# Kernel optimization log

Measured on AMD Instinct MI355X. Metric: run time of the kernel, lower is better.

## Reference

```python
import jax, jax.numpy as jnp
import numpy as np

N = 20000       # nodes
E = 320000      # edges (before self-loops)
F_IN = 128
HID = 128
HEADS = 4
OUT_DIM = 2
B = 64          # graphs in batch
SLOPE = 0.2     # GATv2 leaky_relu negative slope (PyG default)


def _glorot(key, shape):
    fan_in, fan_out = shape[0], shape[1]
    limit = np.sqrt(6.0 / (fan_in + fan_out)).astype(np.float32)
    return jax.random.uniform(key, shape, jnp.float32, -limit, limit)


def setup_inputs() -> dict:
    key = jax.random.key(0)
    ks = jax.random.split(key, 24)
    inp = {
        'x': jax.random.normal(ks[0], (N, F_IN), jnp.float32),
        'edge_src': jax.random.randint(ks[1], (E,), 0, N),
        'edge_dst': jax.random.randint(ks[2], (E,), 0, N),
        'batch': jnp.sort(jax.random.randint(ks[3], (N,), 0, B)),
        # layer 1: in=F_IN, out=HEADS*HID, concat
        'Wl1': _glorot(ks[4], (F_IN, HEADS * HID)),
        'Wr1': _glorot(ks[5], (F_IN, HEADS * HID)),
        'bl1': jnp.zeros((HEADS * HID,), jnp.float32),
        'br1': jnp.zeros((HEADS * HID,), jnp.float32),
        'att1': _glorot(ks[6], (HEADS, HID)),
        'bias1': jnp.zeros((HEADS * HID,), jnp.float32),
        # layer 2: in=HEADS*HID, out=HEADS*HID, concat
        'Wl2': _glorot(ks[7], (HEADS * HID, HEADS * HID)),
        'Wr2': _glorot(ks[8], (HEADS * HID, HEADS * HID)),
        'bl2': jnp.zeros((HEADS * HID,), jnp.float32),
        'br2': jnp.zeros((HEADS * HID,), jnp.float32),
        'att2': _glorot(ks[9], (HEADS, HID)),
        'bias2': jnp.zeros((HEADS * HID,), jnp.float32),
        # layer 3: in=HEADS*HID, heads=1, concat=False -> out=HID
        'Wl3': _glorot(ks[10], (HEADS * HID, HID)),
        'Wr3': _glorot(ks[11], (HEADS * HID, HID)),
        'bl3': jnp.zeros((HID,), jnp.float32),
        'br3': jnp.zeros((HID,), jnp.float32),
        'att3': _glorot(ks[12], (1, HID)),
        'bias3': jnp.zeros((HID,), jnp.float32),
        # output MLP
        'W_mlp1': _glorot(ks[13], (HID, HID)),
        'b_mlp1': jnp.zeros((HID,), jnp.float32),
        'W_mlp2': _glorot(ks[14], (HID, OUT_DIM)),
        'b_mlp2': jnp.zeros((OUT_DIM,), jnp.float32),
    }
    return inp


def gatv2_layer(x, src, dst, Wl, Wr, bl, br, att, bias, concat):
    """PyG GATv2Conv (eval mode): alpha_ij = softmax_j over N(i) of a^T LeakyReLU(xl_j + xr_i)."""
    H, C = att.shape
    n = x.shape[0]
    xl = (x @ Wl + bl).reshape(n, H, C)   # source transform
    e = jax.nn.leaky_relu(xl[src] + (x @ Wr + br).reshape(n, H, C)[dst], SLOPE)  # [E,H,C]
    logits = jnp.einsum('ehc,hc->eh', e, att)                                    # [E,H]
    # segment softmax over destination node
    m = jax.ops.segment_max(logits, dst, num_segments=n)
    alpha = jnp.exp(logits - m[dst])
    denom = jax.ops.segment_sum(alpha, dst, num_segments=n)
    alpha = alpha / denom[dst]
    out = jax.ops.segment_sum(xl[src] * alpha[..., None], dst, num_segments=n)   # [N,H,C]
    out = out.reshape(n, H * C) if concat else out.mean(axis=1)
    return out + bias


def reference(x, edge_src, edge_dst, batch,
              Wl1, Wr1, bl1, br1, att1, bias1,
              Wl2, Wr2, bl2, br2, att2, bias2,
              Wl3, Wr3, bl3, br3, att3, bias3,
              W_mlp1, b_mlp1, W_mlp2, b_mlp2):
    n = x.shape[0]
    loop = jnp.arange(n, dtype=edge_src.dtype)
    src = jnp.concatenate([edge_src, loop])   # PyG add_self_loops=True
    dst = jnp.concatenate([edge_dst, loop])

    h = jax.nn.elu(gatv2_layer(x, src, dst, Wl1, Wr1, bl1, br1, att1, bias1, True))
    h = jax.nn.elu(gatv2_layer(h, src, dst, Wl2, Wr2, bl2, br2, att2, bias2, True))
    h = jax.nn.elu(gatv2_layer(h, src, dst, Wl3, Wr3, bl3, br3, att3, bias3, False))

    # global_mean_pool over graph ids
    counts = jnp.maximum(jax.ops.segment_sum(jnp.ones((n,), h.dtype), batch, num_segments=B), 1.0)
    pooled = jax.ops.segment_sum(h, batch, num_segments=B) / counts[:, None]

    hidden = jax.nn.relu(pooled @ W_mlp1 + b_mlp1)
    return hidden @ W_mlp2 + b_mlp2
```

## Files before the change

### kernel.cpp

```cpp
#include <hip/hip_runtime.h>
#include <math.h>


typedef __attribute__((ext_vector_type(4))) float f32x4;
typedef __attribute__((ext_vector_type(8))) _Float16 f16x8;
typedef __attribute__((ext_vector_type(4))) _Float16 f16x4;
typedef __attribute__((ext_vector_type(2))) _Float16 f16x2;

__device__ __forceinline__ float elu1(float x) {
    return (x > 0.f) ? x : (__expf(x) - 1.f);
}
__device__ __forceinline__ f16x2 pk_leaky(f16x2 s) {
    const f16x2 slope = {(_Float16)0.2f, (_Float16)0.2f};
    return __builtin_elementwise_max(s, s * slope);
}

__global__ void zero32_kernel(int* __restrict__ p, int n) {
    int i = blockIdx.x * 256 + threadIdx.x;
    if (i < n) p[i] = 0;
}

__global__ void count_kernel(const int* __restrict__ dst, int* __restrict__ cnt,
                             int E, int N) {
    int e = blockIdx.x * 256 + threadIdx.x;
    if (e < E + N) {
        int d = (e < E) ? dst[e] : (e - E);
        atomicAdd(&cnt[d], 1);
    }
}

__global__ __launch_bounds__(1024) void scan_kernel(const int* __restrict__ cnt,
                                                    int* __restrict__ rowstart,
                                                    int* __restrict__ cursor,
                                                    int N, int total) {
    __shared__ int part[1024];
    int t = threadIdx.x;
    int ch = (N + 1023) >> 10;
    int base = t * ch;
    int loc[32];
    int s = 0;
    for (int i = 0; i < ch && i < 32; ++i) {
        int idx = base + i;
        int v = (idx < N) ? cnt[idx] : 0;
        loc[i] = s;
        s += v;
    }
    part[t] = s;
    __syncthreads();
    for (int off = 1; off < 1024; off <<= 1) {
        int v = (t >= off) ? part[t - off] : 0;
        __syncthreads();
        part[t] += v;
        __syncthreads();
    }
    int excl = (t == 0) ? 0 : part[t - 1];
    for (int i = 0; i < ch && i < 32; ++i) {
        int idx = base + i;
        if (idx < N) {
            int v = excl + loc[i];
            rowstart[idx] = v;
            cursor[idx]   = v;
        }
    }
    if (t == 0) rowstart[N] = total;
}

__global__ void scatter_kernel(const int* __restrict__ src, const int* __restrict__ dst,
                               int* __restrict__ cursor, int* __restrict__ csr_src,
                               int E, int N) {
    int e = blockIdx.x * 256 + threadIdx.x;
    if (e < E + N) {
        int d, s;
        if (e < E) { d = dst[e]; s = src[e]; }
        else       { d = e - E; s = e - E; }
        int pos = atomicAdd(&cursor[d], 1);
        csr_src[pos] = s;
    }
}

__global__ void boundary_kernel(const int* __restrict__ batch,
                                int* __restrict__ gstart, int N, int B) {
    int n = blockIdx.x * 256 + threadIdx.x;
    if (n > N) return;
    int cur  = (n < N) ? batch[n] : B;
    int prev = (n == 0) ? -1 : batch[n - 1];
    for (int g = prev + 1; g <= cur; ++g) gstart[g] = n;
}

__global__ void convA_kernel(const float* __restrict__ X, _Float16* __restrict__ A,
                             int n_valid, int n_total) {
    int i = (blockIdx.x * 256 + threadIdx.x) * 4;
    if (i >= n_total) return;
    float4 v = (i < n_valid) ? *(const float4*)(X + i) : make_float4(0.f, 0.f, 0.f, 0.f);
    f16x4 h;
    h.x = (_Float16)v.x; h.y = (_Float16)v.y;
    h.z = (_Float16)v.z; h.w = (_Float16)v.w;
    *(f16x4*)(A + i) = h;
}

__global__ __launch_bounds__(256) void convWT_kernel(
    const float* __restrict__ Wl, const float* __restrict__ Wr,
    _Float16* __restrict__ Bth, _Float16* __restrict__ Btl, int K, int Nh) {
    __shared__ float tile[32][33];
    int kb = blockIdx.x * 32;
    int nb = blockIdx.y * 32;
    int tx = threadIdx.x;
    int ty = threadIdx.y;
#pragma unroll
    for (int j = 0; j < 4; ++j) {
        int kk = kb + ty + j * 8;
        int nn = nb + tx;
        float v = (nn < Nh) ? Wl[(size_t)kk * Nh + nn]
                            : Wr[(size_t)kk * Nh + (nn - Nh)];
        tile[ty + j * 8][tx] = v;
    }
    __syncthreads();
#pragma unroll
    for (int j = 0; j < 4; ++j) {
        int nn = nb + ty + j * 8;
        int kk = kb + tx;
        float v = tile[tx][ty + j * 8];
        _Float16 h = (_Float16)v;
        Bth[(size_t)nn * K + kk] = h;
        Btl[(size_t)nn * K + kk] = (_Float16)(v - (float)h);
    }
}

#define SCW 132
__global__ __launch_bounds__(256, 1) void gemm_f16_kernel(
    const _Float16* __restrict__ A,
    const _Float16* __restrict__ Bh, const _Float16* __restrict__ Bl,
    const float* __restrict__ biasL, const float* __restrict__ biasR, int Nh_,
    _Float16* __restrict__ P, _Float16* __restrict__ Q, int K, int NT) {
    __shared__ __align__(16) char smem[49152];
    float* sC = (float*)(smem);

    const int tid  = threadIdx.x;
    const int lane = tid & 63;
    const int wv   = tid >> 6;
    const int wm   = wv & 1;
    const int wn   = wv >> 1;
    const int fm   = lane & 15;
    const int q    = lane >> 4;

    const int bi = blockIdx.x;
    const int kx = bi & 7;
    const int tt = bi >> 3;
    const int m0 = ((tt / NT) * 8 + kx) * 128;
    const int n0 = (tt % NT) * 128;

    const int r0  = lane >> 2;
    const int kco = (lane & 3) << 3;

    f32x4 acc[4][4];
#pragma unroll
    for (int i = 0; i < 4; ++i)
#pragma unroll
        for (int j = 0; j < 4; ++j) {
            acc[i][j].x = 0.f; acc[i][j].y = 0.f;
            acc[i][j].z = 0.f; acc[i][j].w = 0.f;
        }

    const int nIters = K >> 5;
    int cur = 0;
    {
        char* base = smem;
#pragma unroll
        for (int j = 0; j < 2; ++j) {
            int wc  = wv * 2 + j;
            int row = wc * 16 + r0;
            size_t ga = (size_t)(m0 + row) * K + kco;
            size_t gb = (size_t)(n0 + row) * K + kco;
            int lofs = wc * 1024;
            __builtin_amdgcn_global_load_lds(
                (const __attribute__((address_space(1))) void*)(A + ga),
                (__attribute__((address_space(3))) void*)(base + lofs), 16, 0, 0);
            __builtin_amdgcn_global_load_lds(
                (const __attribute__((address_space(1))) void*)(Bh + gb),
                (__attribute__((address_space(3))) void*)(base + 8192 + lofs), 16, 0, 0);
            __builtin_amdgcn_global_load_lds(
                (const __attribute__((address_space(1))) void*)(Bl + gb),
                (__attribute__((address_space(3))) void*)(base + 16384 + lofs), 16, 0, 0);
        }
    }
    for (int it = 0; it < nIters; ++it) {
        __syncthreads();
        if (it + 1 < nIters) {
            char* base = smem + (cur ^ 1) * 24576;
            int ks = (it + 1) << 5;
#pragma unroll
            for (int j = 0; j < 2; ++j) {
                int wc  = wv * 2 + j;
                int row = wc * 16 + r0;
                size_t ga = (size_t)(m0 + row) * K + ks + kco;
                size_t gb = (size_t)(n0 + row) * K + ks + kco;
                int lofs = wc * 1024;
                __builtin_amdgcn_global_load_lds(
                    (const __attribute__((address_space(1))) void*)(A + ga),
                    (__attribute__((address_space(3))) void*)(base + lofs), 16, 0, 0);
                __builtin_amdgcn_global_load_lds(
                    (const __attribute__((address_space(1))) void*)(Bh + gb),
                    (__attribute__((address_space(3))) void*)(base + 8192 + lofs), 16, 0, 0);
                __builtin_amdgcn_global_load_lds(
                    (const __attribute__((address_space(1))) void*)(Bl + gb),
                    (__attribute__((address_space(3))) void*)(base + 16384 + lofs), 16, 0, 0);
            }
        }

        _Float16* cA  = (_Float16*)(smem + cur * 24576);
        _Float16* cBh = (_Float16*)(smem + cur * 24576 + 8192);
        _Float16* cBl = (_Float16*)(smem + cur * 24576 + 16384);
        f16x8 ah[4];
#pragma unroll
        for (int mi = 0; mi < 4; ++mi)
            ah[mi] = *(const f16x8*)&cA[(wm * 64 + mi * 16 + fm) * 32 + q * 8];
#pragma unroll
        for (int ni = 0; ni < 4; ++ni) {
            int r = (wn * 64 + ni * 16 + fm) * 32 + q * 8;
            f16x8 bh = *(const f16x8*)&cBh[r];
            f16x8 bl = *(const f16x8*)&cBl[r];
#pragma unroll
            for (int mi = 0; mi < 4; ++mi) {
                acc[mi][ni] = __builtin_amdgcn_mfma_f32_16x16x32_f16(ah[mi], bh, acc[mi][ni], 0, 0, 0);
                acc[mi][ni] = __builtin_amdgcn_mfma_f32_16x16x32_f16(ah[mi], bl, acc[mi][ni], 0, 0, 0);
            }
        }
        cur ^= 1;
    }

    float bsv[4];
#pragma unroll
    for (int ni = 0; ni < 4; ++ni) {
        int col = n0 + wn * 64 + ni * 16 + fm;
        bsv[ni] = (col < Nh_) ? biasL[col] : biasR[col - Nh_];
    }

    _Float16* dstbase = (n0 < Nh_) ? P : Q;
    const int col0 = (n0 < Nh_) ? n0 : (n0 - Nh_);

#pragma unroll
    for (int c = 0; c < 2; ++c) {
        __syncthreads();
        if (wm == c) {
#pragma unroll
            for (int mi = 0; mi < 4; ++mi)
#pragma unroll
                for (int ni = 0; ni < 4; ++ni) {
                    int base = (mi * 16 + q * 4) * SCW + wn * 64 + ni * 16 + fm;
                    sC[base]           = acc[mi][ni].x + bsv[ni];
                    sC[base + SCW]     = acc[mi][ni].y + bsv[ni];
                    sC[base + 2 * SCW] = acc[mi][ni].z + bsv[ni];
                    sC[base + 3 * SCW] = acc[mi][ni].w + bsv[ni];
                }
        }
        __syncthreads();
#pragma unroll
        for (int j = 0; j < 8; ++j) {
            int flat = j * 256 + tid;
            int row  = flat >> 5;
            int col  = (flat & 31) * 4;
            f32x4 v = *(const f32x4*)(sC + row * SCW + col);
            f16x4 hv;
            hv.x = (_Float16)v.x; hv.y = (_Float16)v.y;
            hv.z = (_Float16)v.z; hv.w = (_Float16)v.w;
            *(f16x4*)(dstbase + (size_t)(m0 + c * 64 + row) * Nh_ + col0 + col) = hv;
        }
    }
}

__global__ __launch_bounds__(256) void gat_edge4_kernel(
    const _Float16* __restrict__ P, const _Float16* __restrict__ Q,
    const float* __restrict__ att, const float* __restrict__ bias,
    const int* __restrict__ rowstart, const int* __restrict__ srcs,
    _Float16* __restrict__ H, int N) {
    __shared__ float s_l[4][4];
    __shared__ float s_acc[4][512];

    int n = blockIdx.x;
    int wv = threadIdx.x >> 6;
    int lane = threadIdx.x & 63;
    int c0 = lane * 8;
    int h = lane >> 4;

    f16x8 rv = *(const f16x8*)(Q + (size_t)n * 512 + c0);
    f16x2 r2[4], t2[4];
#pragma unroll
    for (int k = 0; k < 4; ++k) {
        r2[k].x = rv[2 * k]; r2[k].y = rv[2 * k + 1];
        t2[k].x = (_Float16)att[c0 + 2 * k];
        t2[k].y = (_Float16)att[c0 + 2 * k + 1];
    }

    float acc[8];
#pragma unroll
    for (int j = 0; j < 8; ++j) acc[j] = 0.f;
    float l_run = 0.f;

    int beg = rowstart[n], end = rowstart[n + 1];
    int i = beg + wv * 2;
    for (; i + 1 < end; i += 8) {
        int s0 = srcs[i];
        int s1 = srcs[i + 1];
        f16x8 hv0 = *(const f16x8*)(P + (size_t)s0 * 512 + c0);
        f16x8 hv1 = *(const f16x8*)(P + (size_t)s1 * 512 + c0);
        float p0 = 0.f, p1 = 0.f;
#pragma unroll
        for (int k = 0; k < 4; ++k) {
            f16x2 a0; a0.x = hv0[2 * k]; a0.y = hv0[2 * k + 1];
            f16x2 a1; a1.x = hv1[2 * k]; a1.y = hv1[2 * k + 1];
            p0 = __builtin_amdgcn_fdot2(pk_leaky(a0 + r2[k]), t2[k], p0, false);
            p1 = __builtin_amdgcn_fdot2(pk_leaky(a1 + r2[k]), t2[k], p1, false);
        }
        p0 += __shfl_xor(p0, 1, 16);
        p1 += __shfl_xor(p1, 1, 16);
        p0 += __shfl_xor(p0, 2, 16);
        p1 += __shfl_xor(p1, 2, 16);
        p0 += __shfl_xor(p0, 4, 16);
        p1 += __shfl_xor(p1, 4, 16);
        p0 += __shfl_xor(p0, 8, 16);
        p1 += __shfl_xor(p1, 8, 16);
        float w0 = __expf(p0);
        float w1 = __expf(p1);
        l_run += w0 + w1;
#pragma unroll
        for (int j = 0; j < 8; ++j) {
            float a = fmaf((float)hv0[j], w0, acc[j]);
            acc[j] = fmaf((float)hv1[j], w1, a);
        }
    }
    if (i < end) {
        int s = srcs[i];
        f16x8 hv = *(const f16x8*)(P + (size_t)s * 512 + c0);
        float p = 0.f;
#pragma unroll
        for (int k = 0; k < 4; ++k) {
            f16x2 a; a.x = hv[2 * k]; a.y = hv[2 * k + 1];
            p = __builtin_amdgcn_fdot2(pk_leaky(a + r2[k]), t2[k], p, false);
        }
        p += __shfl_xor(p, 1, 16);
        p += __shfl_xor(p, 2, 16);
        p += __shfl_xor(p, 4, 16);
        p += __shfl_xor(p, 8, 16);
        float w = __expf(p);
        l_run += w;
#pragma unroll
        for (int j = 0; j < 8; ++j)
            acc[j] = fmaf((float)hv[j], w, acc[j]);
    }
    if ((lane & 15) == 0) s_l[wv][h] = l_run;
    *(float4*)&s_acc[wv][c0]     = make_float4(acc[0], acc[1], acc[2], acc[3]);
    *(float4*)&s_acc[wv][c0 + 4] = make_float4(acc[4], acc[5], acc[6], acc[7]);
    __syncthreads();
    if (wv == 0) {
        float L = s_l[0][h] + s_l[1][h] + s_l[2][h] + s_l[3][h];
        float o[8];
#pragma unroll
        for (int j = 0; j < 8; ++j) o[j] = 0.f;
#pragma unroll
        for (int w = 0; w < 4; ++w) {
            float4 q0 = *(const float4*)&s_acc[w][c0];
            float4 q1 = *(const float4*)&s_acc[w][c0 + 4];
            o[0] += q0.x; o[1] += q0.y; o[2] += q0.z; o[3] += q0.w;
            o[4] += q1.x; o[5] += q1.y; o[6] += q1.z; o[7] += q1.w;
        }
        float inv = 1.f / L;
        f16x8 oh;
#pragma unroll
        for (int j = 0; j < 8; ++j)
            oh[j] = (_Float16)elu1(o[j] * inv + bias[c0 + j]);
        *(f16x8*)(H + (size_t)n * 512 + c0) = oh;
    }
}

__global__ __launch_bounds__(256) void gat_edge1_kernel(
    const _Float16* __restrict__ P, const _Float16* __restrict__ Q,
    const float* __restrict__ att, const float* __restrict__ bias,
    const int* __restrict__ rowstart, const int* __restrict__ srcs,
    float* __restrict__ out, int N) {
    __shared__ float s_l[4];
    __shared__ float s_acc[4][128];

    int n = blockIdx.x;
    int wv = threadIdx.x >> 6;
    int lane = threadIdx.x & 63;
    int c0 = lane * 2;

    f16x2 rv = *(const f16x2*)(Q + (size_t)n * 128 + c0);
    f16x2 t2;
    t2.x = (_Float16)att[c0];
    t2.y = (_Float16)att[c0 + 1];

    float acc0 = 0.f, acc1 = 0.f;
    float l_run = 0.f;

    int beg = rowstart[n], end = rowstart[n + 1];
    int i = beg + wv * 2;
    for (; i + 1 < end; i += 8) {
        int s0 = srcs[i];
        int s1 = srcs[i + 1];
        f16x2 h0 = *(const f16x2*)(P + (size_t)s0 * 128 + c0);
        f16x2 h1 = *(const f16x2*)(P + (size_t)s1 * 128 + c0);
        float p0 = __builtin_amdgcn_fdot2(pk_leaky(h0 + rv), t2, 0.f, false);
        float p1 = __builtin_amdgcn_fdot2(pk_leaky(h1 + rv), t2, 0.f, false);
        p0 += __shfl_xor(p0, 1, 64);
        p1 += __shfl_xor(p1, 1, 64);
        p0 += __shfl_xor(p0, 2, 64);
        p1 += __shfl_xor(p1, 2, 64);
        p0 += __shfl_xor(p0, 4, 64);
        p1 += __shfl_xor(p1, 4, 64);
        p0 += __shfl_xor(p0, 8, 64);
        p1 += __shfl_xor(p1, 8, 64);
        p0 += __shfl_xor(p0, 16, 64);
        p1 += __shfl_xor(p1, 16, 64);
        p0 += __shfl_xor(p0, 32, 64);
        p1 += __shfl_xor(p1, 32, 64);
        float w0 = __expf(p0);
        float w1 = __expf(p1);
        l_run += w0 + w1;
        acc0 = fmaf((float)h1.x, w1, fmaf((float)h0.x, w0, acc0));
        acc1 = fmaf((float)h1.y, w1, fmaf((float)h0.y, w0, acc1));
    }
    if (i < end) {
        int s = srcs[i];
        f16x2 hv = *(const f16x2*)(P + (size_t)s * 128 + c0);
        float p = __builtin_amdgcn_fdot2(pk_leaky(hv + rv), t2, 0.f, false);
        p += __shfl_xor(p, 1, 64);
        p += __shfl_xor(p, 2, 64);
        p += __shfl_xor(p, 4, 64);
        p += __shfl_xor(p, 8, 64);
        p += __shfl_xor(p, 16, 64);
        p += __shfl_xor(p, 32, 64);
        float w = __expf(p);
        l_run += w;
        acc0 = fmaf((float)hv.x, w, acc0);
        acc1 = fmaf((float)hv.y, w, acc1);
    }
    if (lane == 0) s_l[wv] = l_run;
    *(float2*)&s_acc[wv][c0] = make_float2(acc0, acc1);
    __syncthreads();
    if (wv == 0) {
        float L = s_l[0] + s_l[1] + s_l[2] + s_l[3];
        float o0 = 0.f, o1 = 0.f;
#pragma unroll
        for (int w = 0; w < 4; ++w) {
            float2 qv = *(const float2*)&s_acc[w][c0];
            o0 += qv.x;
            o1 += qv.y;
        }
        float inv = 1.f / L;
        float2 w2;
        w2.x = elu1(o0 * inv + bias[c0]);
        w2.y = elu1(o1 * inv + bias[c0 + 1]);
        *(float2*)(out + (size_t)n * 128 + c0) = w2;
    }
}

__global__ __launch_bounds__(256) void pool2_kernel(
    const float* __restrict__ h3, const int* __restrict__ gstart,
    float* __restrict__ pooled) {
    __shared__ float red[256];
    int g = blockIdx.x;
    int c = threadIdx.x & 127;
    int h = threadIdx.x >> 7;
    int gs = gstart[g], ge = gstart[g + 1];
    float s = 0.f;
    for (int n = gs + h; n < ge; n += 2) s += h3[(size_t)n * 128 + c];
    red[threadIdx.x] = s;
    __syncthreads();
    if (h == 0) {
        float tot = red[c] + red[c + 128];
        float cnt = fmaxf((float)(ge - gs), 1.f);
        pooled[g * 128 + c] = tot / cnt;
    }
}

__global__ __launch_bounds__(128) void mlp_kernel(
    const float* __restrict__ pooled,
    const float* __restrict__ W1, const float* __restrict__ b1,
    const float* __restrict__ W2, const float* __restrict__ b2,
    float* __restrict__ out) {
    __shared__ float pr[128];
    __shared__ float2 red[128];
    int g = blockIdx.x;
    int t = threadIdx.x;
    pr[t] = pooled[g * 128 + t];
    __syncthreads();
    float h = b1[t];
#pragma unroll 4
    for (int k = 0; k < 128; ++k) h = fmaf(pr[k], W1[k * 128 + t], h);
    h = fmaxf(h, 0.0f);
    red[t] = make_float2(h * W2[t * 2], h * W2[t * 2 + 1]);
    __syncthreads();
    for (int s = 64; s > 0; s >>= 1) {
        if (t < s) {
            red[t].x += red[t + s].x;
            red[t].y += red[t + s].y;
        }
        __syncthreads();
    }
    if (t == 0) {
        out[g * 2]     = red[0].x + b2[0];
        out[g * 2 + 1] = red[0].y + b2[1];
    }
}

extern "C" void kernel_launch(void* const* d_in, const int* in_sizes, int n_in,
                              void* d_out, int out_size, void* d_ws, size_t ws_size,
                              hipStream_t stream) {
    const float* x     = (const float*)d_in[0];
    const int*   esrc  = (const int*)d_in[1];
    const int*   edst  = (const int*)d_in[2];
    const int*   batch = (const int*)d_in[3];
    const float* Wl1   = (const float*)d_in[4];
    const float* Wr1   = (const float*)d_in[5];
    const float* bl1   = (const float*)d_in[6];
    const float* br1   = (const float*)d_in[7];
    const float* att1  = (const float*)d_in[8];
    const float* bias1 = (const float*)d_in[9];
    const float* Wl2   = (const float*)d_in[10];
    const float* Wr2   = (const float*)d_in[11];
    const float* bl2   = (const float*)d_in[12];
    const float* br2   = (const float*)d_in[13];
    const float* att2  = (const float*)d_in[14];
    const float* bias2 = (const float*)d_in[15];
    const float* Wl3   = (const float*)d_in[16];
    const float* Wr3   = (const float*)d_in[17];
    const float* bl3   = (const float*)d_in[18];
    const float* br3   = (const float*)d_in[19];
    const float* att3  = (const float*)d_in[20];
    const float* bias3 = (const float*)d_in[21];
    const float* Wm1   = (const float*)d_in[22];
    const float* bm1   = (const float*)d_in[23];
    const float* Wm2   = (const float*)d_in[24];
    const float* bm2   = (const float*)d_in[25];

    int N  = in_sizes[0] / 128;
    int E  = in_sizes[1];
    int ET = E + N;
    int B  = out_size / 2;
    const int Mp = 160 * 128;

    char* ws = (char*)d_ws;
    size_t off = 0;
    auto alloc = [&](size_t bytes) -> void* {
        void* p = ws + off;
        off += (bytes + 255) & ~(size_t)255;
        return p;
    };
    _Float16* P    = (_Float16*)alloc((size_t)Mp * 512 * 2);
    _Float16* Q    = (_Float16*)alloc((size_t)Mp * 512 * 2);
    _Float16* A1   = (_Float16*)alloc((size_t)Mp * 128 * 2);
    _Float16* Hb   = (_Float16*)alloc((size_t)Mp * 512 * 2);
    _Float16* Wth1 = (_Float16*)alloc((size_t)1024 * 128 * 2);
    _Float16* Wtl1 = (_Float16*)alloc((size_t)1024 * 128 * 2);
    _Float16* Wth2 = (_Float16*)alloc((size_t)1024 * 512 * 2);
    _Float16* Wtl2 = (_Float16*)alloc((size_t)1024 * 512 * 2);
    _Float16* Wth3 = (_Float16*)alloc((size_t)256 * 512 * 2);
    _Float16* Wtl3 = (_Float16*)alloc((size_t)256 * 512 * 2);
    float*    R3   = (float*)alloc((size_t)Mp * 128 * 4);
    int*    cnt      = (int*)alloc((size_t)N * 4);
    int*    rowstart = (int*)alloc((size_t)(N + 1) * 4);
    int*    cursor   = (int*)alloc((size_t)N * 4);
    int*    csr_src  = (int*)alloc((size_t)ET * 4);
    int*    gstart   = (int*)alloc((size_t)(B + 1) * 4);
    float*  pooled   = (float*)alloc((size_t)B * 128 * 4);
    (void)ws_size;

    zero32_kernel<<<(N + 255) / 256, 256, 0, stream>>>(cnt, N);

    count_kernel<<<(ET + 255) / 256, 256, 0, stream>>>(edst, cnt, E, N);
    scan_kernel<<<1, 1024, 0, stream>>>(cnt, rowstart, cursor, N, ET);
    scatter_kernel<<<(ET + 255) / 256, 256, 0, stream>>>(esrc, edst, cursor, csr_src, E, N);
    boundary_kernel<<<(N + 256) / 256, 256, 0, stream>>>(batch, gstart, N, B);

    convWT_kernel<<<dim3(4, 32),  dim3(32, 8), 0, stream>>>(Wl1, Wr1, Wth1, Wtl1, 128, 512);
    convWT_kernel<<<dim3(16, 32), dim3(32, 8), 0, stream>>>(Wl2, Wr2, Wth2, Wtl2, 512, 512);
    convWT_kernel<<<dim3(16, 8),  dim3(32, 8), 0, stream>>>(Wl3, Wr3, Wth3, Wtl3, 512, 128);

    convA_kernel<<<((Mp * 128 / 4) + 255) / 256, 256, 0, stream>>>(x, A1, N * 128, Mp * 128);

    gemm_f16_kernel<<<160 * 8, 256, 0, stream>>>(A1, Wth1, Wtl1, bl1, br1, 512, P, Q, 128, 8);
    gat_edge4_kernel<<<N, 256, 0, stream>>>(P, Q, att1, bias1, rowstart, csr_src, Hb, N);

    gemm_f16_kernel<<<160 * 8, 256, 0, stream>>>(Hb, Wth2, Wtl2, bl2, br2, 512, P, Q, 512, 8);
    gat_edge4_kernel<<<N, 256, 0, stream>>>(P, Q, att2, bias2, rowstart, csr_src, Hb, N);

    gemm_f16_kernel<<<160 * 2, 256, 0, stream>>>(Hb, Wth3, Wtl3, bl3, br3, 128, P, Q, 512, 2);
    gat_edge1_kernel<<<N, 256, 0, stream>>>(P, Q, att3, bias3, rowstart, csr_src, R3, N);

    pool2_kernel<<<B, 256, 0, stream>>>(R3, gstart, pooled);
    mlp_kernel<<<B, 128, 0, stream>>>(pooled, Wm1, bm1, Wm2, bm2, (float*)d_out);
}
```

Before: 444.3 us.

## Assign one wavefront per destination node in edge kernels and parallelize CSR scan

The GAT edge kernels now map each destination node to one 64-lane wavefront (four nodes per block) instead of splitting a node's edges across four wavefronts. This removes the shared-memory cross-wave reduction and the __syncthreads, and stops three of four waves idling in the epilogue. Each node's edges are now walked serially by one wave, so per-node latency grows. The single-block 1024-thread scan is replaced by a three-kernel block-reduce / serial-prefix / block-scan, which adds two launches but spreads the scan across many blocks.

```diff
diff --git a/kernel.cpp b/kernel.cpp
--- a/kernel.cpp
+++ b/kernel.cpp
@@ -29,40 +29,45 @@
     }
 }
 
-__global__ __launch_bounds__(1024) void scan_kernel(const int* __restrict__ cnt,
+__global__ __launch_bounds__(256) void scan1_kernel(const int* __restrict__ cnt,
+                                                    int* __restrict__ psum, int N) {
+    __shared__ int red[256];
+    int idx = blockIdx.x * 256 + threadIdx.x;
+    red[threadIdx.x] = (idx < N) ? cnt[idx] : 0;
+    __syncthreads();
+    for (int s = 128; s > 0; s >>= 1) {
+        if (threadIdx.x < s) red[threadIdx.x] += red[threadIdx.x + s];
+        __syncthreads();
+    }
+    if (threadIdx.x == 0) psum[blockIdx.x] = red[0];
+}
+__global__ void scan2_kernel(int* __restrict__ psum, int nch) {
+    if (threadIdx.x == 0) {
+        int run = 0;
+        for (int i = 0; i < nch; ++i) { int v = psum[i]; psum[i] = run; run += v; }
+    }
+}
+__global__ __launch_bounds__(256) void scan3_kernel(const int* __restrict__ cnt,
+                                                    const int* __restrict__ psum,
                                                     int* __restrict__ rowstart,
-                                                    int* __restrict__ cursor,
-                                                    int N, int total) {
-    __shared__ int part[1024];
-    int t = threadIdx.x;
-    int ch = (N + 1023) >> 10;
-    int base = t * ch;
-    int loc[32];
-    int s = 0;
-    for (int i = 0; i < ch && i < 32; ++i) {
-        int idx = base + i;
-        int v = (idx < N) ? cnt[idx] : 0;
-        loc[i] = s;
-        s += v;
-    }
-    part[t] = s;
+                                                    int* __restrict__ cursor, int N) {
+    __shared__ int buf[256];
+    int idx = blockIdx.x * 256 + threadIdx.x;
+    int v = (idx < N) ? cnt[idx] : 0;
+    buf[threadIdx.x] = v;
     __syncthreads();
-    for (int off = 1; off < 1024; off <<= 1) {
-        int v = (t >= off) ? part[t - off] : 0;
-        __syncthreads();
-        part[t] += v;
-        __syncthreads();
-    }
-    int excl = (t == 0) ? 0 : part[t - 1];
-    for (int i = 0; i < ch && i < 32; ++i) {
-        int idx = base + i;
-        if (idx < N) {
-            int v = excl + loc[i];
-            rowstart[idx] = v;
-            cursor[idx]   = v;
-        }
-    }
-    if (t == 0) rowstart[N] = total;
+    for (int off = 1; off < 256; off <<= 1) {
+        int t = (threadIdx.x >= off) ? buf[threadIdx.x - off] : 0;
+        __syncthreads();
+        buf[threadIdx.x] += t;
+        __syncthreads();
+    }
+    int excl = buf[threadIdx.x] - v + psum[blockIdx.x];
+    if (idx < N) {
+        rowstart[idx] = excl;
+        cursor[idx]   = excl;
+        if (idx == N - 1) rowstart[N] = excl + v;
+    }
 }
 
 __global__ void scatter_kernel(const int* __restrict__ src, const int* __restrict__ dst,
@@ -273,14 +278,11 @@
     const float* __restrict__ att, const float* __restrict__ bias,
     const int* __restrict__ rowstart, const int* __restrict__ srcs,
     _Float16* __restrict__ H, int N) {
-    __shared__ float s_l[4][4];
-    __shared__ float s_acc[4][512];
-
-    int n = blockIdx.x;
     int wv = threadIdx.x >> 6;
     int lane = threadIdx.x & 63;
+    int n = blockIdx.x * 4 + wv;
+    if (n >= N) return;
     int c0 = lane * 8;
-    int h = lane >> 4;
 
     f16x8 rv = *(const f16x8*)(Q + (size_t)n * 512 + c0);
     f16x2 r2[4], t2[4];
@@ -297,8 +299,8 @@
     float l_run = 0.f;
 
     int beg = rowstart[n], end = rowstart[n + 1];
-    int i = beg + wv * 2;
-    for (; i + 1 < end; i += 8) {
+    int i = beg;
+    for (; i + 1 < end; i += 2) {
         int s0 = srcs[i];
         int s1 = srcs[i + 1];
         f16x8 hv0 = *(const f16x8*)(P + (size_t)s0 * 512 + c0);
@@ -347,29 +349,12 @@
         for (int j = 0; j < 8; ++j)
             acc[j] = fmaf((float)hv[j], w, acc[j]);
     }
-    if ((lane & 15) == 0) s_l[wv][h] = l_run;
-    *(float4*)&s_acc[wv][c0]     = make_float4(acc[0], acc[1], acc[2], acc[3]);
-    *(float4*)&s_acc[wv][c0 + 4] = make_float4(acc[4], acc[5], acc[6], acc[7]);
-    __syncthreads();
-    if (wv == 0) {
-        float L = s_l[0][h] + s_l[1][h] + s_l[2][h] + s_l[3][h];
-        float o[8];
-#pragma unroll
-        for (int j = 0; j < 8; ++j) o[j] = 0.f;
-#pragma unroll
-        for (int w = 0; w < 4; ++w) {
-            float4 q0 = *(const float4*)&s_acc[w][c0];
-            float4 q1 = *(const float4*)&s_acc[w][c0 + 4];
-            o[0] += q0.x; o[1] += q0.y; o[2] += q0.z; o[3] += q0.w;
-            o[4] += q1.x; o[5] += q1.y; o[6] += q1.z; o[7] += q1.w;
-        }
-        float inv = 1.f / L;
-        f16x8 oh;
-#pragma unroll
-        for (int j = 0; j < 8; ++j)
-            oh[j] = (_Float16)elu1(o[j] * inv + bias[c0 + j]);
-        *(f16x8*)(H + (size_t)n * 512 + c0) = oh;
-    }
+    float inv = 1.f / l_run;
+    f16x8 oh;
+#pragma unroll
+    for (int j = 0; j < 8; ++j)
+        oh[j] = (_Float16)elu1(acc[j] * inv + bias[c0 + j]);
+    *(f16x8*)(H + (size_t)n * 512 + c0) = oh;
 }
 
 __global__ __launch_bounds__(256) void gat_edge1_kernel(
@@ -377,12 +362,10 @@
     const float* __restrict__ att, const float* __restrict__ bias,
     const int* __restrict__ rowstart, const int* __restrict__ srcs,
     float* __restrict__ out, int N) {
-    __shared__ float s_l[4];
-    __shared__ float s_acc[4][128];
-
-    int n = blockIdx.x;
     int wv = threadIdx.x >> 6;
     int lane = threadIdx.x & 63;
+    int n = blockIdx.x * 4 + wv;
+    if (n >= N) return;
     int c0 = lane * 2;
 
     f16x2 rv = *(const f16x2*)(Q + (size_t)n * 128 + c0);
@@ -394,8 +377,8 @@
     float l_run = 0.f;
 
     int beg = rowstart[n], end = rowstart[n + 1];
-    int i = beg + wv * 2;
-    for (; i + 1 < end; i += 8) {
+    int i = beg;
+    for (; i + 1 < end; i += 2) {
         int s0 = srcs[i];
         int s1 = srcs[i + 1];
         f16x2 h0 = *(const f16x2*)(P + (size_t)s0 * 128 + c0);
@@ -435,24 +418,11 @@
         acc0 = fmaf((float)hv.x, w, acc0);
         acc1 = fmaf((float)hv.y, w, acc1);
     }
-    if (lane == 0) s_l[wv] = l_run;
-    *(float2*)&s_acc[wv][c0] = make_float2(acc0, acc1);
-    __syncthreads();
-    if (wv == 0) {
-        float L = s_l[0] + s_l[1] + s_l[2] + s_l[3];
-        float o0 = 0.f, o1 = 0.f;
-#pragma unroll
-        for (int w = 0; w < 4; ++w) {
-            float2 qv = *(const float2*)&s_acc[w][c0];
-            o0 += qv.x;
-            o1 += qv.y;
-        }
-        float inv = 1.f / L;
-        float2 w2;
-        w2.x = elu1(o0 * inv + bias[c0]);
-        w2.y = elu1(o1 * inv + bias[c0 + 1]);
-        *(float2*)(out + (size_t)n * 128 + c0) = w2;
-    }
+    float inv = 1.f / l_run;
+    float2 w2;
+    w2.x = elu1(acc0 * inv + bias[c0]);
+    w2.y = elu1(acc1 * inv + bias[c0 + 1]);
+    *(float2*)(out + (size_t)n * 128 + c0) = w2;
 }
 
 __global__ __launch_bounds__(256) void pool2_kernel(
@@ -539,6 +509,7 @@
     int ET = E + N;
     int B  = out_size / 2;
     const int Mp = 160 * 128;
+    int nch = (N + 255) / 256;
 
     char* ws = (char*)d_ws;
     size_t off = 0;
@@ -559,6 +530,7 @@
     _Float16* Wtl3 = (_Float16*)alloc((size_t)256 * 512 * 2);
     float*    R3   = (float*)alloc((size_t)Mp * 128 * 4);
     int*    cnt      = (int*)alloc((size_t)N * 4);
+    int*    psum     = (int*)alloc((size_t)(nch + 1) * 4);
     int*    rowstart = (int*)alloc((size_t)(N + 1) * 4);
     int*    cursor   = (int*)alloc((size_t)N * 4);
     int*    csr_src  = (int*)alloc((size_t)ET * 4);
@@ -569,7 +541,9 @@
     zero32_kernel<<<(N + 255) / 256, 256, 0, stream>>>(cnt, N);
 
     count_kernel<<<(ET + 255) / 256, 256, 0, stream>>>(edst, cnt, E, N);
-    scan_kernel<<<1, 1024, 0, stream>>>(cnt, rowstart, cursor, N, ET);
+    scan1_kernel<<<nch, 256, 0, stream>>>(cnt, psum, N);
+    scan2_kernel<<<1, 64, 0, stream>>>(psum, nch);
+    scan3_kernel<<<nch, 256, 0, stream>>>(cnt, psum, rowstart, cursor, N);
     scatter_kernel<<<(ET + 255) / 256, 256, 0, stream>>>(esrc, edst, cursor, csr_src, E, N);
     boundary_kernel<<<(N + 256) / 256, 256, 0, stream>>>(batch, gstart, N, B);
 
@@ -579,14 +553,16 @@
 
     convA_kernel<<<((Mp * 128 / 4) + 255) / 256, 256, 0, stream>>>(x, A1, N * 128, Mp * 128);
 
+    int eblocks = (N + 3) / 4;
+
     gemm_f16_kernel<<<160 * 8, 256, 0, stream>>>(A1, Wth1, Wtl1, bl1, br1, 512, P, Q, 128, 8);
-    gat_edge4_kernel<<<N, 256, 0, stream>>>(P, Q, att1, bias1, rowstart, csr_src, Hb, N);
+    gat_edge4_kernel<<<eblocks, 256, 0, stream>>>(P, Q, att1, bias1, rowstart, csr_src, Hb, N);
 
     gemm_f16_kernel<<<160 * 8, 256, 0, stream>>>(Hb, Wth2, Wtl2, bl2, br2, 512, P, Q, 512, 8);
-    gat_edge4_kernel<<<N, 256, 0, stream>>>(P, Q, att2, bias2, rowstart, csr_src, Hb, N);
+    gat_edge4_kernel<<<eblocks, 256, 0, stream>>>(P, Q, att2, bias2, rowstart, csr_src, Hb, N);
 
     gemm_f16_kernel<<<160 * 2, 256, 0, stream>>>(Hb, Wth3, Wtl3, bl3, br3, 128, P, Q, 512, 2);
-    gat_edge1_kernel<<<N, 256, 0, stream>>>(P, Q, att3, bias3, rowstart, csr_src, R3, N);
+    gat_edge1_kernel<<<eblocks, 256, 0, stream>>>(P, Q, att3, bias3, rowstart, csr_src, R3, N);
 
     pool2_kernel<<<B, 256, 0, stream>>>(R3, gstart, pooled);
     mlp_kernel<<<B, 128, 0, stream>>>(pooled, Wm1, bm1, Wm2, bm2, (float*)d_out);
```

Result: faster. 433.9 us (-2.3%).
